# Optimization experiments

Hardware: AMD Instinct MI355X
Metric: run time of the kernel (lower is better)

Reference implementation:

```python
import jax, jax.numpy as jnp
import numpy as np

B, N, H, F = 4, 256, 192, 64
SUP = 1.0  # ancestor_suppression_strength
EPS = 1e-6


def setup_inputs() -> dict:
    key = jax.random.key(0)
    ks = jax.random.split(key, 14)
    z = jax.random.normal(ks[0], (B, H), jnp.float32)
    # strictly-lower-triangular 0/1 parent (link) matrix: row t lists parents j < t
    tri = jnp.tril(jnp.ones((N, N), jnp.float32), -1)
    targets = (jax.random.uniform(ks[1], (B, N, N)) < 0.05).astype(jnp.float32) * tri

    def w(k, shape):
        fan_in = shape[0]
        return jax.random.normal(k, shape, jnp.float32) / jnp.sqrt(jnp.float32(fan_in))

    return {
        "z": z,
        "teacher_forcing_targets": targets,
        "W_init": w(ks[2], (H, H)), "b_init": jnp.zeros((H,), jnp.float32),
        "W_ih": w(ks[3], (H, 3 * H)), "W_hh": w(ks[4], (H, 3 * H)),
        "b_ih": jnp.zeros((3 * H,), jnp.float32), "b_hh": jnp.zeros((3 * H,), jnp.float32),
        "W1": w(ks[5], (3 * H, H)), "b1": jnp.zeros((H,), jnp.float32),
        "W2": w(ks[6], (H, 1)), "b2": jnp.zeros((1,), jnp.float32),
        "Wf": w(ks[7], (H, F)), "bf": jnp.zeros((F,), jnp.float32),
        "atom_count": N,
    }


def gru_cell(x, h, W_ih, W_hh, b_ih, b_hh):
    gx = x @ W_ih + b_ih
    gh = h @ W_hh + b_hh
    xr, xu, xn = jnp.split(gx, 3, axis=-1)
    hr, hu, hn = jnp.split(gh, 3, axis=-1)
    r = jax.nn.sigmoid(xr + hr)
    u = jax.nn.sigmoid(xu + hu)
    n = jnp.tanh(xn + r * hn)
    return (1.0 - u) * n + u * h


def reference(z, teacher_forcing_targets, W_init, b_init, W_ih, W_hh, b_ih, b_hh,
              W1, b1, W2, b2, Wf, bf, atom_count):
    b, n = teacher_forcing_targets.shape[0], teacher_forcing_targets.shape[1]
    h = z.shape[-1]
    idx = jnp.arange(n)

    # decoder_init: latent z -> hidden state of node 0
    h0 = jnp.tanh(z @ W_init + b_init)
    S0 = jnp.zeros((b, n, h), z.dtype).at[:, 0].set(h0)   # node states
    A0 = jnp.zeros((b, n, n), z.dtype)                    # ancestor indicator A[b,i,j]=1 iff j ancestor of i

    def step(carry, xs):
        S, A, ll = carry
        t, tgt = xs                                   # t scalar, tgt (B,N) = parents of node t
        mask = (idx < t).astype(S.dtype)              # existing nodes
        cnt = jnp.maximum(mask.sum(), 1.0)
        # mean-aggregation over existing node states -> GRU message
        m = (S * mask[None, :, None]).sum(axis=1) / cnt              # (B,H)
        h_prov = gru_cell(m, z, W_ih, W_hh, b_ih, b_hh)              # provisional state of new node
        # parent logits: MLP([h_new, h_existing, z]) per candidate parent
        feats = jnp.concatenate([
            jnp.broadcast_to(h_prov[:, None, :], S.shape), S,
            jnp.broadcast_to(z[:, None, :], S.shape)], axis=-1)      # (B,N,3H)
        logits = (jax.nn.relu(feats @ W1 + b1) @ W2 + b2)[..., 0]    # (B,N)
        # ancestor suppression: suppress j if j is already an ancestor of one of t's parents
        reach = jnp.einsum('bn,bnm->bm', tgt, A)
        anc = (reach > 0).astype(S.dtype)
        p = jax.nn.sigmoid(logits) * (1.0 - SUP * anc)
        p = jnp.clip(p, EPS, 1.0 - EPS)
        ll = ll + (mask[None, :] * (tgt * jnp.log(p) + (1.0 - tgt) * jnp.log1p(-p))).sum()
        # teacher forcing: commit parents, update new-node state from parent states
        deg = jnp.maximum(tgt.sum(axis=-1, keepdims=True), 1.0)
        msg = jnp.einsum('bn,bnh->bh', tgt, S) / deg
        h_new = gru_cell(msg, h_prov, W_ih, W_hh, b_ih, b_hh)
        S = jax.lax.dynamic_update_slice(S, h_new[:, None, :], (0, t, 0))
        row = jnp.minimum(tgt + anc, 1.0)             # ancestors(t) = parents U ancestors(parents)
        A = jax.lax.dynamic_update_slice(A, row[:, None, :], (0, t, 0))
        return (S, A, ll), None

    ts = jnp.arange(1, n)
    tgt_rows = jnp.swapaxes(teacher_forcing_targets[:, 1:, :], 0, 1)  # (N-1,B,N)
    (S, A, ll), _ = jax.lax.scan(step, (S0, A0, jnp.zeros((), z.dtype)), (ts, tgt_rows))

    L = teacher_forcing_targets            # teacher-forced link matrix
    node_features = S @ Wf + bf            # node_feature_decoder head
    return L, node_features, ll
```

## Files before the change

kernel.cpp:

```cpp
#include <hip/hip_runtime.h>
#include <stdint.h>

#define B_ 4
#define N_ 256
#define H_ 192
#define H3_ 576
#define F_ 64
#define SH_ 12
#define SC_ 36

#define H0_OFF   0u
#define ZC_OFF   1024u
#define HL_OFF   2048u
#define SL_OFF   395264u
#define AN_OFF   788480u
#define TG_OFF   796672u
#define PL_OFF   804864u
#define PC_OFF   870400u
#define DG_OFF   871424u
#define G_OFF    872448u
#define C_OFF    1069056u
#define CL_OFF   1265664u
#define CC_OFF   1331200u
#define XC_OFF   1332224u
#define FHL_OFF  1332288u
#define FSL_OFF  1725504u

#define AN64 (AN_OFF/2)
#define TG64 (TG_OFF/2)

#define NF_OUT 262144u
#define LL_OUT 327680u

__device__ __forceinline__ float sigm_(float x){ return 1.0f/(1.0f + __expf(-x)); }
__device__ __forceinline__ float tanh_(float x){
  float ax = fabsf(x);
  float e = __expf(-2.0f*ax);
  float t = (1.0f - e)/(1.0f + e);
  return x < 0.0f ? -t : t;
}

__device__ __forceinline__ void st_mall_(uint32_t* p, unsigned long long u){
  __hip_atomic_store((unsigned long long*)p, u, __ATOMIC_RELAXED, __HIP_MEMORY_SCOPE_AGENT);
}
__device__ __forceinline__ unsigned long long ld_mall_(const uint32_t* p){
  return __hip_atomic_load((const unsigned long long*)p, __ATOMIC_RELAXED, __HIP_MEMORY_SCOPE_AGENT);
}
__device__ __forceinline__ unsigned long long ld_l2_(const uint32_t* p){
  unsigned long long v;
  asm volatile("buffer_inv sc0\n\t"
               "s_waitcnt vmcnt(0)\n\t"
               "global_load_dwordx2 %0, %1, off\n\t"
               "s_waitcnt vmcnt(0)"
               : "=v"(v) : "v"(p) : "memory");
  return v;
}
__device__ __forceinline__ void pub_(uint32_t* fp, uint32_t* mp, float v, uint32_t tag){
  unsigned long long u = ((unsigned long long)tag<<32) | (unsigned long long)__float_as_uint(v);
  __hip_atomic_store((unsigned long long*)fp, u, __ATOMIC_RELAXED, __HIP_MEMORY_SCOPE_WORKGROUP);
  st_mall_(mp, u);
}
__device__ __forceinline__ float pollH_(const uint32_t* fp, const uint32_t* mp, int fast, uint32_t tag){
  unsigned long long x = 0; int it = 0;
  for(;;){
    if (fast){
      x = ld_l2_(fp);
      if ((uint32_t)(x>>32) != tag && (((++it) & 3) == 3)){
        unsigned long long m = ld_mall_(mp);
        if ((uint32_t)(m>>32) == tag) x = m;
      }
    } else {
      x = ld_mall_(mp);
    }
    if (__all((int)((uint32_t)(x>>32) == tag))) break;
  }
  return __uint_as_float((uint32_t)x);
}

__global__ void __launch_bounds__(192) k_pre1(const float* __restrict__ z,
    const float* __restrict__ Winit, const float* __restrict__ binit,
    const float* __restrict__ W1, const float* __restrict__ b1,
    const float* __restrict__ tgt, float* ws, float* out)
{
  int bx = blockIdx.x, b = blockIdx.y, tid = threadIdx.x;
  if (bx == N_){
    __shared__ float zs[H_];
    zs[tid] = z[b*H_ + tid];
    __syncthreads();
    float a0=0.f, a1=0.f;
    for (int k=0;k<H_;k++){
      float zv = zs[k];
      a0 += zv * Winit[(size_t)k*H_ + tid];
      a1 += zv * W1[(size_t)(2*H_ + k)*H_ + tid];
    }
    ws[H0_OFF + b*H_ + tid] = tanh_(a0 + binit[tid]);
    ws[ZC_OFF + b*H_ + tid] = a1 + b1[tid];
    if (b==0 && tid==0) out[LL_OUT] = 0.0f;
    return;
  }
  if (tid >= 64) return;
  int t = bx, lane = tid;
  uint32_t* wsu = (uint32_t*)ws;
  unsigned long long* ws64 = (unsigned long long*)ws;
  const float* row = tgt + ((size_t)(b*N_) + t)*N_;
  uint8_t* pl = ((uint8_t*)&wsu[PL_OFF]) + (size_t)(b*N_ + t)*N_;
  int cnt = 0;
  #pragma unroll
  for (int m=0;m<4;m++){
    float v = row[m*64 + lane];
    bool p = (v != 0.0f);
    unsigned long long bw = __ballot(p);
    if (lane == 0) ws64[TG64 + (size_t)(b*N_+t)*4 + m] = bw;
    if (p){
      int pos = cnt + (int)__popcll(bw & ((1ULL<<lane)-1ULL));
      pl[pos] = (uint8_t)(m*64 + lane);
    }
    cnt += (int)__popcll(bw);
  }
  if (lane == 0){
    wsu[PC_OFF + b*N_ + t] = (uint32_t)cnt;
    ws[DG_OFF + b*N_ + t] = 1.0f / fmaxf((float)cnt, 1.0f);
  }
}

__global__ void __launch_bounds__(64) k_pre2(float* ws)
{
  int j = blockIdx.x, b = blockIdx.y, lane = threadIdx.x;
  uint32_t* wsu = (uint32_t*)ws;
  unsigned long long* ws64 = (unsigned long long*)ws;
  uint8_t* cl = ((uint8_t*)&wsu[CL_OFF]) + (size_t)(b*N_ + j)*N_;
  int w = j >> 6; int sb = j & 63;
  int cnt = 0;
  #pragma unroll
  for (int m=0;m<4;m++){
    int t = m*64 + lane;
    unsigned long long rowm = ws64[TG64 + (size_t)(b*N_+t)*4 + w];
    bool p = ((rowm >> sb) & 1ULL) != 0ULL;
    unsigned long long bw = __ballot(p);
    if (p){
      int pos = cnt + (int)__popcll(bw & ((1ULL<<lane)-1ULL));
      cl[pos] = (uint8_t)t;
    }
    cnt += (int)__popcll(bw);
  }
  if (lane == 0) wsu[CC_OFF + b*N_ + j] = (uint32_t)cnt;
}

__global__ void __launch_bounds__(256) k_pass1(const float* __restrict__ z,
    const float* __restrict__ Wih, const float* __restrict__ Whh,
    const float* __restrict__ bih_g, const float* __restrict__ bhh_g,
    float* ws)
{
  int bx = blockIdx.x;
  int b = bx & 7;
  if (b >= B_) return;
  int slice = bx >> 3;
  int tid = threadIdx.x;
  float* wsf = ws;
  uint32_t* wsu = (uint32_t*)ws;
  unsigned long long* ws64 = (unsigned long long*)ws;

  __shared__ __align__(16) float sruns[H_];
  __shared__ __align__(16) float sh[H_];
  __shared__ __align__(16) float sPS[N_*SC_];
  __shared__ __align__(16) float sdelta[2][SC_];
  __shared__ int sfast[16];
  __shared__ unsigned long long sAB[N_][4];
  __shared__ float sDG[N_], sTF1[N_], sTF2[N_];

  const int hh = tid >> 4;
  const int kc = tid & 15;
  const bool mv = tid < 192;

  uint32_t xcc = (uint32_t)__builtin_amdgcn_s_getreg((31u<<11) | 20u) & 15u;
  if (tid == 0)
    __hip_atomic_store(&wsu[XC_OFF + b*16 + slice], 0xC0DE0000u | xcc,
                       __ATOMIC_RELAXED, __HIP_MEMORY_SCOPE_AGENT);
  if (tid < 64){
    uint32_t v = 0; int ok;
    do {
      v = (tid < 16) ? __hip_atomic_load(&wsu[XC_OFF + b*16 + tid],
              __ATOMIC_RELAXED, __HIP_MEMORY_SCOPE_AGENT) : 0xC0DE0000u;
      ok = (int)((v >> 16) == 0xC0DEu);
    } while (!__all(ok));
    if (tid < 16) sfast[tid] = ((v & 0xFFu) == xcc) ? 1 : 0;
  }

  for (int i = tid; i < N_; i += 256){
    sDG[i] = wsf[DG_OFF + b*N_ + i];
    float f1 = 0.f, f2 = 0.f;
    if (i >= 1){
      unsigned long long w1 = ws64[TG64 + (size_t)(b*N_+i)*4 + ((i-1)>>6)];
      f1 = (float)((w1 >> ((i-1)&63)) & 1ULL);
    }
    if (i >= 2){
      unsigned long long w2 = ws64[TG64 + (size_t)(b*N_+i)*4 + ((i-2)>>6)];
      f2 = (float)((w2 >> ((i-2)&63)) & 1ULL);
    }
    sTF1[i] = f1; sTF2[i] = f2;
  }

  float rwih[3][12], rwhh[3][12], rbih[3], rbhh[3], rghz[3];
  if (mv){
    #pragma unroll
    for (int g=0; g<3; g++){
      int col = g*H_ + slice*SH_ + hh;
      #pragma unroll
      for (int i=0;i<12;i++){
        rwih[g][i] = Wih[(size_t)(kc*12+i)*H3_ + col];
        rwhh[g][i] = Whh[(size_t)(kc*12+i)*H3_ + col];
      }
      rbih[g] = bih_g[col];
      rbhh[g] = bhh_g[col];
    }
    float a0=0.f,a1=0.f,a2=0.f;
    #pragma unroll
    for (int i=0;i<12;i++){
      float zv = z[b*H_ + kc*12 + i];
      a0 += zv*rwhh[0][i]; a1 += zv*rwhh[1][i]; a2 += zv*rwhh[2][i];
    }
    #pragma unroll
    for (int m=1;m<16;m<<=1){
      a0 += __shfl_xor(a0,m); a1 += __shfl_xor(a1,m); a2 += __shfl_xor(a2,m);
    }
    rghz[0]=a0+rbhh[0]; rghz[1]=a1+rbhh[1]; rghz[2]=a2+rbhh[2];
  }
  float zreg = mv ? z[b*H_ + slice*SH_ + hh] : 0.0f;
  for (int i = tid; i < N_*SC_; i += 256) sPS[i] = 0.0f;
  if (tid >= 192 && tid < 196) sAB[0][tid-192] = 0ULL;
  if (mv && kc == 0){
    float v = wsf[H0_OFF + b*H_ + slice*SH_ + hh];
    int e = slice*SH_ + hh;
    pub_(&wsu[FSL_OFF + (unsigned)(b*N_)*384u + 2u*e],
         &wsu[SL_OFF  + (unsigned)(b*N_)*384u + 2u*e], v, 1u);
  }
  __syncthreads();

  const int fastf = mv ? sfast[tid/12] : 0;
  float rsum = 0.f;
  float qp0=0.f,qp1=0.f,qp2=0.f, dp0=0.f,dp1=0.f,dp2=0.f;

  for (int t=1; t<N_; t++){
    const uint32_t tagS = (uint32_t)t;
    const uint32_t tagH = (uint32_t)(t+1);
    if (mv){
      float v = pollH_(&wsu[FSL_OFF + (unsigned)(b*N_+(t-1))*384u + 2u*(unsigned)tid],
                       &wsu[SL_OFF  + (unsigned)(b*N_+(t-1))*384u + 2u*(unsigned)tid],
                       fastf, tagS);
      rsum += v;
      sruns[tid] = rsum;
    }
    __syncthreads();
    float hp=0.f, a20=0.f, a21=0.f, a22=0.f;
    if (mv){
      float dginv = sDG[t], tf1 = sTF1[t], tf2 = sTF2[t];
      float x[12];
      *(float4*)&x[0] = *(float4*)&sruns[kc*12];
      *(float4*)&x[4] = *(float4*)&sruns[kc*12+4];
      *(float4*)&x[8] = *(float4*)&sruns[kc*12+8];
      float q0=0.f,q1=0.f,q2=0.f;
      #pragma unroll
      for (int i=0;i<12;i++){
        q0 += x[i]*rwih[0][i]; q1 += x[i]*rwih[1][i]; q2 += x[i]*rwih[2][i];
      }
      #pragma unroll
      for (int m=1;m<16;m<<=1){
        q0 += __shfl_xor(q0,m); q1 += __shfl_xor(q1,m); q2 += __shfl_xor(q2,m);
      }
      float d0=q0-qp0, d1=q1-qp1, d2=q2-qp2;
      qp0=q0; qp1=q1; qp2=q2;
      if (kc == 0){
        sdelta[t&1][0*12+hh]=d0; sdelta[t&1][1*12+hh]=d1; sdelta[t&1][2*12+hh]=d2;
      }
      float pv0 = sPS[t*SC_ + 0*12 + hh];
      float pv1 = sPS[t*SC_ + 1*12 + hh];
      float pv2 = sPS[t*SC_ + 2*12 + hh];
      a20 = (pv0 + tf1*d0 + tf2*dp0)*dginv + rbih[0];
      a21 = (pv1 + tf1*d1 + tf2*dp1)*dginv + rbih[1];
      a22 = (pv2 + tf1*d2 + tf2*dp2)*dginv + rbih[2];
      dp0=d0; dp1=d1; dp2=d2;
      float invt = 1.0f/(float)t;
      float a10 = q0*invt + rbih[0];
      float a11 = q1*invt + rbih[1];
      float a12 = q2*invt + rbih[2];
      float r = sigm_(a10 + rghz[0]);
      float u = sigm_(a11 + rghz[1]);
      float n = tanh_(a12 + r*rghz[2]);
      hp = (1.0f-u)*n + u*zreg;
      if (kc == 0){
        int e = slice*SH_ + hh;
        pub_(&wsu[FHL_OFF + (unsigned)(b*N_+t)*384u + 2u*e],
             &wsu[HL_OFF  + (unsigned)(b*N_+t)*384u + 2u*e], hp, tagH);
      }
      float hv = pollH_(&wsu[FHL_OFF + (unsigned)(b*N_+t)*384u + 2u*(unsigned)tid],
                        &wsu[HL_OFF  + (unsigned)(b*N_+t)*384u + 2u*(unsigned)tid],
                        fastf, tagH);
      sh[tid] = hv;
    } else {
      int lane = tid - 192;
      if (lane < SC_){
        if (t >= 2){
          int node = t-2;
          int ccn = (int)wsu[CC_OFF + b*N_ + node];
          const uint8_t* cl = ((const uint8_t*)&wsu[CL_OFF]) + (size_t)(b*N_ + node)*N_;
          float dd = sdelta[(t-1)&1][lane];
          for (int i=0;i<ccn;i++){
            int tc = cl[i];
            if (tc > t) sPS[tc*SC_ + lane] += dd;
          }
        }
      } else if (lane < SC_+4){
        int w = lane - SC_;
        int npt = (int)wsu[PC_OFF + b*N_ + t];
        const uint8_t* pb = ((const uint8_t*)&wsu[PL_OFF]) + (size_t)(b*N_ + t)*N_;
        unsigned long long acc = 0ULL;
        for (int i=0;i<npt;i++) acc |= sAB[pb[i]][w];
        if (slice == 0) ws64[AN64 + (size_t)(b*N_+t)*4 + w] = acc;
        sAB[t][w] = acc | ws64[TG64 + (size_t)(b*N_+t)*4 + w];
      }
    }
    __syncthreads();
    if (mv){
      float x[12];
      *(float4*)&x[0] = *(float4*)&sh[kc*12];
      *(float4*)&x[4] = *(float4*)&sh[kc*12+4];
      *(float4*)&x[8] = *(float4*)&sh[kc*12+8];
      float y0=0.f,y1=0.f,y2=0.f;
      #pragma unroll
      for (int i=0;i<12;i++){
        y0 += x[i]*rwhh[0][i]; y1 += x[i]*rwhh[1][i]; y2 += x[i]*rwhh[2][i];
      }
      #pragma unroll
      for (int m=1;m<16;m<<=1){
        y0 += __shfl_xor(y0,m); y1 += __shfl_xor(y1,m); y2 += __shfl_xor(y2,m);
      }
      float r2 = sigm_(a20 + y0 + rbhh[0]);
      float u2 = sigm_(a21 + y1 + rbhh[1]);
      float n2 = tanh_(a22 + r2*(y2 + rbhh[2]));
      float hn = (1.0f-u2)*n2 + u2*hp;
      if (kc == 0){
        int e = slice*SH_ + hh;
        pub_(&wsu[FSL_OFF + (unsigned)(b*N_+t)*384u + 2u*e],
             &wsu[SL_OFF  + (unsigned)(b*N_+t)*384u + 2u*e], hn, tagH);
      }
    }
  }
}

__global__ void k_p2a(const float* __restrict__ W1, const float* __restrict__ Wf,
    const float* __restrict__ bf, float* ws, float* out)
{
  int j = blockIdx.x, b = blockIdx.y, tid = threadIdx.x;
  __shared__ float srow[H_], hrow[H_];
  __shared__ float nfp[3][F_];
  srow[tid] = ws[SL_OFF + (unsigned)(b*N_+j)*384u + 2u*tid];
  hrow[tid] = ws[HL_OFF + (unsigned)(b*N_+j)*384u + 2u*tid];
  __syncthreads();
  float accG = 0.f, accC = 0.f;
  for (int k=0;k<H_;k++){
    float sv = srow[k], hv = hrow[k];
    accG += sv * W1[(size_t)(H_+k)*H_ + tid];
    accC += hv * W1[(size_t)k*H_ + tid];
  }
  ws[G_OFF + ((size_t)b*H_ + tid)*N_ + j] = accG;
  ws[C_OFF + (size_t)(b*N_+j)*H_ + tid] = accC + ws[ZC_OFF + b*H_ + tid];
  int f = tid & 63, kp = tid >> 6;
  float a = 0.f;
  for (int i=0;i<64;i++){ int k = kp*64 + i; a += srow[k]*Wf[(size_t)k*F_ + f]; }
  nfp[kp][f] = a;
  __syncthreads();
  if (tid < F_) out[NF_OUT + (size_t)(b*N_+j)*F_ + tid] = nfp[0][tid]+nfp[1][tid]+nfp[2][tid] + bf[tid];
}

__global__ void __launch_bounds__(256) k_p2b(const float* __restrict__ W2,
    const float* __restrict__ b2p, float* ws, float* out)
{
  int t = blockIdx.x + 1, b = blockIdx.y;
  int tid = threadIdx.x; int lane = tid & 63; int wv = tid >> 6;
  __shared__ float cv[H_], w2s[H_];
  __shared__ float wsum[4];
  unsigned long long* ws64 = (unsigned long long*)ws;
  if (tid < H_){
    cv[tid] = ws[C_OFF + (size_t)(b*N_+t)*H_ + tid];
    w2s[tid] = W2[tid];
  }
  __syncthreads();
  float acc = 0.f;
  if (tid < t){
    const float* GT = ws + G_OFF + (size_t)b*H_*N_;
    float a = 0.f;
    for (int k=0;k<H_;k++) a += fmaxf(cv[k] + GT[(size_t)k*N_ + tid], 0.f) * w2s[k];
    float logit = a + b2p[0];
    float pp = 1.0f/(1.0f+__expf(-logit));
    unsigned long long an = ws64[AN64 + (size_t)(b*N_+t)*4 + (tid>>6)];
    unsigned long long tg = ws64[TG64 + (size_t)(b*N_+t)*4 + (tid>>6)];
    float anc = (float)((an >> (tid&63)) & 1ULL);
    pp = pp * (1.0f - anc);
    pp = fminf(fmaxf(pp, 1e-6f), 1.0f - 1e-6f);
    int tgb = (int)((tg >> (tid&63)) & 1ULL);
    acc = tgb ? logf(pp) : log1pf(-pp);
  }
  #pragma unroll
  for (int m=32;m>=1;m>>=1) acc += __shfl_xor(acc, m);
  if (lane == 0) wsum[wv] = acc;
  __syncthreads();
  if (tid == 0) atomicAdd(out + LL_OUT, wsum[0]+wsum[1]+wsum[2]+wsum[3]);
}

extern "C" void kernel_launch(void* const* d_in, const int* in_sizes, int n_in,
                              void* d_out, int out_size, void* d_ws, size_t ws_size,
                              hipStream_t stream) {
  (void)in_sizes; (void)n_in; (void)out_size; (void)ws_size;
  const float* z     = (const float*)d_in[0];
  const float* tgt   = (const float*)d_in[1];
  const float* Winit = (const float*)d_in[2];
  const float* binit = (const float*)d_in[3];
  const float* Wih   = (const float*)d_in[4];
  const float* Whh   = (const float*)d_in[5];
  const float* bih   = (const float*)d_in[6];
  const float* bhh   = (const float*)d_in[7];
  const float* W1    = (const float*)d_in[8];
  const float* b1    = (const float*)d_in[9];
  const float* W2    = (const float*)d_in[10];
  const float* b2    = (const float*)d_in[11];
  const float* Wf    = (const float*)d_in[12];
  const float* bf    = (const float*)d_in[13];
  float* out = (float*)d_out;
  float* ws  = (float*)d_ws;

  hipMemcpyAsync(d_out, d_in[1], (size_t)B_*N_*N_*sizeof(float), hipMemcpyDeviceToDevice, stream);

  k_pre1<<<dim3(N_+1, B_), dim3(192), 0, stream>>>(z, Winit, binit, W1, b1, tgt, ws, out);
  k_pre2<<<dim3(N_, B_), dim3(64), 0, stream>>>(ws);
  k_pass1<<<dim3(128), dim3(256), 0, stream>>>(z, Wih, Whh, bih, bhh, ws);
  k_p2a<<<dim3(N_, B_), dim3(H_), 0, stream>>>(W1, Wf, bf, ws, out);
  k_p2b<<<dim3(N_-1, B_), dim3(256), 0, stream>>>(W2, b2, ws, out);
}
```

Before: 930.0 us.

## Repartition GRU recurrence across three blocks per batch with per-step delta gather

The sequential recurrence kernel goes from 16 blocks per batch element (12 hidden units each, 256 threads) to 3 blocks per batch element (64 hidden units each, 512 threads), which cuts the number of blocks that must exchange state through global memory every step. The old scatter of prefix-sum deltas into shared memory, and the k_pre2 child-list kernel that fed it, are removed. In their place each step writes its delta rows to global memory, and the parent-message term is built by gathering those rows over the parent list. Each block now publishes and polls only the other blocks' slices, and the ancestor OR-reduction is split across 16 lanes. The cost is more registers per thread (24-wide weight slices), a per-step global gather over parents, and fewer CUs doing the serial work.

```diff
diff --git a/kernel.cpp b/kernel.cpp
--- a/kernel.cpp
+++ b/kernel.cpp
@@ -6,8 +6,6 @@
 #define H_ 192
 #define H3_ 576
 #define F_ 64
-#define SH_ 12
-#define SC_ 36
 
 #define H0_OFF   0u
 #define ZC_OFF   1024u
@@ -18,13 +16,12 @@
 #define PL_OFF   804864u
 #define PC_OFF   870400u
 #define DG_OFF   871424u
-#define G_OFF    872448u
-#define C_OFF    1069056u
-#define CL_OFF   1265664u
-#define CC_OFF   1331200u
-#define XC_OFF   1332224u
-#define FHL_OFF  1332288u
-#define FSL_OFF  1725504u
+#define D_OFF    872448u
+#define G_OFF    1462272u
+#define C_OFF    1658880u
+#define FHL_OFF  1855488u
+#define FSL_OFF  2248704u
+#define XC_OFF   2641920u
 
 #define AN64 (AN_OFF/2)
 #define TG64 (TG_OFF/2)
@@ -123,30 +120,7 @@
   }
 }
 
-__global__ void __launch_bounds__(64) k_pre2(float* ws)
-{
-  int j = blockIdx.x, b = blockIdx.y, lane = threadIdx.x;
-  uint32_t* wsu = (uint32_t*)ws;
-  unsigned long long* ws64 = (unsigned long long*)ws;
-  uint8_t* cl = ((uint8_t*)&wsu[CL_OFF]) + (size_t)(b*N_ + j)*N_;
-  int w = j >> 6; int sb = j & 63;
-  int cnt = 0;
-  #pragma unroll
-  for (int m=0;m<4;m++){
-    int t = m*64 + lane;
-    unsigned long long rowm = ws64[TG64 + (size_t)(b*N_+t)*4 + w];
-    bool p = ((rowm >> sb) & 1ULL) != 0ULL;
-    unsigned long long bw = __ballot(p);
-    if (p){
-      int pos = cnt + (int)__popcll(bw & ((1ULL<<lane)-1ULL));
-      cl[pos] = (uint8_t)t;
-    }
-    cnt += (int)__popcll(bw);
-  }
-  if (lane == 0) wsu[CC_OFF + b*N_ + j] = (uint32_t)cnt;
-}
-
-__global__ void __launch_bounds__(256) k_pass1(const float* __restrict__ z,
+__global__ void __launch_bounds__(512, 2) k_pass1(const float* __restrict__ z,
     const float* __restrict__ Wih, const float* __restrict__ Whh,
     const float* __restrict__ bih_g, const float* __restrict__ bhh_g,
     float* ws)
@@ -154,196 +128,194 @@
   int bx = blockIdx.x;
   int b = bx & 7;
   if (b >= B_) return;
-  int slice = bx >> 3;
+  int blk = bx >> 3;
   int tid = threadIdx.x;
+  const int e  = tid >> 3;
+  const int kc = tid & 7;
+  const int E  = blk*64 + e;
+
   float* wsf = ws;
   uint32_t* wsu = (uint32_t*)ws;
   unsigned long long* ws64 = (unsigned long long*)ws;
 
-  __shared__ __align__(16) float sruns[H_];
   __shared__ __align__(16) float sh[H_];
-  __shared__ __align__(16) float sPS[N_*SC_];
-  __shared__ __align__(16) float sdelta[2][SC_];
-  __shared__ int sfast[16];
+  __shared__ __align__(16) float ss[H_];
+  __shared__ float sDG[N_], sTF1[N_];
+  __shared__ uint32_t sPC[N_];
+  __shared__ int sfast[4];
   __shared__ unsigned long long sAB[N_][4];
-  __shared__ float sDG[N_], sTF1[N_], sTF2[N_];
-
-  const int hh = tid >> 4;
-  const int kc = tid & 15;
-  const bool mv = tid < 192;
+
+  {
+    float v = wsf[H0_OFF + b*H_ + E];
+    if (kc == 0)
+      pub_(&wsu[FSL_OFF + (unsigned)(b*N_)*384u + 2u*(unsigned)E],
+           &wsu[SL_OFF  + (unsigned)(b*N_)*384u + 2u*(unsigned)E], v, 1u);
+    if (kc == 1) ss[E] = v;
+  }
 
   uint32_t xcc = (uint32_t)__builtin_amdgcn_s_getreg((31u<<11) | 20u) & 15u;
   if (tid == 0)
-    __hip_atomic_store(&wsu[XC_OFF + b*16 + slice], 0xC0DE0000u | xcc,
+    __hip_atomic_store(&wsu[XC_OFF + b*16 + blk], 0xC0DE0000u | xcc,
                        __ATOMIC_RELAXED, __HIP_MEMORY_SCOPE_AGENT);
   if (tid < 64){
     uint32_t v = 0; int ok;
     do {
-      v = (tid < 16) ? __hip_atomic_load(&wsu[XC_OFF + b*16 + tid],
-              __ATOMIC_RELAXED, __HIP_MEMORY_SCOPE_AGENT) : 0xC0DE0000u;
+      v = (tid < 3) ? __hip_atomic_load(&wsu[XC_OFF + b*16 + tid],
+              __ATOMIC_RELAXED, __HIP_MEMORY_SCOPE_AGENT) : (0xC0DE0000u | xcc);
       ok = (int)((v >> 16) == 0xC0DEu);
     } while (!__all(ok));
-    if (tid < 16) sfast[tid] = ((v & 0xFFu) == xcc) ? 1 : 0;
-  }
-
-  for (int i = tid; i < N_; i += 256){
+    if (tid < 3) sfast[tid] = ((v & 0xFFu) == xcc) ? 1 : 0;
+  }
+
+  for (int i = tid; i < N_; i += 512){
     sDG[i] = wsf[DG_OFF + b*N_ + i];
-    float f1 = 0.f, f2 = 0.f;
+    sPC[i] = wsu[PC_OFF + b*N_ + i];
+    float f1 = 0.f;
     if (i >= 1){
       unsigned long long w1 = ws64[TG64 + (size_t)(b*N_+i)*4 + ((i-1)>>6)];
       f1 = (float)((w1 >> ((i-1)&63)) & 1ULL);
     }
-    if (i >= 2){
-      unsigned long long w2 = ws64[TG64 + (size_t)(b*N_+i)*4 + ((i-2)>>6)];
-      f2 = (float)((w2 >> ((i-2)&63)) & 1ULL);
-    }
-    sTF1[i] = f1; sTF2[i] = f2;
-  }
-
-  float rwih[3][12], rwhh[3][12], rbih[3], rbhh[3], rghz[3];
-  if (mv){
-    #pragma unroll
-    for (int g=0; g<3; g++){
-      int col = g*H_ + slice*SH_ + hh;
-      #pragma unroll
-      for (int i=0;i<12;i++){
-        rwih[g][i] = Wih[(size_t)(kc*12+i)*H3_ + col];
-        rwhh[g][i] = Whh[(size_t)(kc*12+i)*H3_ + col];
+    sTF1[i] = f1;
+  }
+  if (blk == 0 && tid >= 192 && tid < 196) sAB[0][tid-192] = 0ULL;
+
+  float rwih[3][24], rwhh[3][24], rbih[3], rbhh[3], rghz[3];
+  #pragma unroll
+  for (int g=0; g<3; g++){
+    int col = g*H_ + E;
+    #pragma unroll
+    for (int i=0;i<24;i++){
+      rwih[g][i] = Wih[(size_t)(kc*24+i)*H3_ + col];
+      rwhh[g][i] = Whh[(size_t)(kc*24+i)*H3_ + col];
+    }
+    rbih[g] = bih_g[col];
+    rbhh[g] = bhh_g[col];
+  }
+  {
+    float a0=0.f,a1=0.f,a2=0.f;
+    #pragma unroll
+    for (int i=0;i<24;i++){
+      float zv = z[b*H_ + kc*24 + i];
+      a0 += zv*rwhh[0][i]; a1 += zv*rwhh[1][i]; a2 += zv*rwhh[2][i];
+    }
+    #pragma unroll
+    for (int m=1;m<8;m<<=1){
+      a0 += __shfl_xor(a0,m); a1 += __shfl_xor(a1,m); a2 += __shfl_xor(a2,m);
+    }
+    rghz[0]=a0+rbhh[0]; rghz[1]=a1+rbhh[1]; rghz[2]=a2+rbhh[2];
+  }
+  float zreg = z[b*H_ + E];
+
+  __syncthreads();
+  if (tid < 128){
+    int j = (tid < blk*64) ? tid : tid + 64;
+    ss[j] = pollH_(&wsu[FSL_OFF + (unsigned)(b*N_)*384u + 2u*(unsigned)j],
+                   &wsu[SL_OFF  + (unsigned)(b*N_)*384u + 2u*(unsigned)j],
+                   sfast[j>>6], 1u);
+  }
+  __syncthreads();
+
+  float q0=0.f, q1=0.f, q2=0.f;
+  const uint8_t* plbase = ((const uint8_t*)&wsu[PL_OFF]) + (size_t)(b*N_)*N_;
+  float* Dbase = wsf + D_OFF + (size_t)((b*3+blk)*N_)*H_;
+
+  for (int t=1; t<N_; t++){
+    const uint32_t tagH = (uint32_t)(t+1);
+    float d0=0.f,d1=0.f,d2=0.f;
+    #pragma unroll
+    for (int c=0;c<6;c++){
+      float4 v4 = *(const float4*)&ss[kc*24 + c*4];
+      float xx0=v4.x, xx1=v4.y, xx2=v4.z, xx3=v4.w;
+      d0 += xx0*rwih[0][c*4+0]; d1 += xx0*rwih[1][c*4+0]; d2 += xx0*rwih[2][c*4+0];
+      d0 += xx1*rwih[0][c*4+1]; d1 += xx1*rwih[1][c*4+1]; d2 += xx1*rwih[2][c*4+1];
+      d0 += xx2*rwih[0][c*4+2]; d1 += xx2*rwih[1][c*4+2]; d2 += xx2*rwih[2][c*4+2];
+      d0 += xx3*rwih[0][c*4+3]; d1 += xx3*rwih[1][c*4+3]; d2 += xx3*rwih[2][c*4+3];
+    }
+    #pragma unroll
+    for (int m=1;m<8;m<<=1){
+      d0 += __shfl_xor(d0,m); d1 += __shfl_xor(d1,m); d2 += __shfl_xor(d2,m);
+    }
+    q0 += d0; q1 += d1; q2 += d2;
+    float invt = 1.0f/(float)t;
+    float r = sigm_(q0*invt + rbih[0] + rghz[0]);
+    float u = sigm_(q1*invt + rbih[1] + rghz[1]);
+    float n = tanh_(q2*invt + rbih[2] + r*rghz[2]);
+    float hp = (1.0f-u)*n + u*zreg;
+    if (kc == 0){
+      pub_(&wsu[FHL_OFF + (unsigned)(b*N_+t)*384u + 2u*(unsigned)E],
+           &wsu[HL_OFF  + (unsigned)(b*N_+t)*384u + 2u*(unsigned)E], hp, tagH);
+      float* Dr = Dbase + (size_t)(t-1)*H_;
+      Dr[e] = d0; Dr[64+e] = d1; Dr[128+e] = d2;
+    }
+    if (kc == 1) sh[E] = hp;
+    float ga0=0.f, ga1=0.f, ga2=0.f;
+    {
+      int pc = (int)sPC[t];
+      const uint8_t* pl = plbase + (size_t)t*N_;
+      for (int i=kc; i<pc; i+=8){
+        int p = pl[i];
+        if (p == t-1) continue;
+        const float* Dp = Dbase + (size_t)p*H_;
+        ga0 += Dp[e]; ga1 += Dp[64+e]; ga2 += Dp[128+e];
       }
-      rbih[g] = bih_g[col];
-      rbhh[g] = bhh_g[col];
-    }
-    float a0=0.f,a1=0.f,a2=0.f;
-    #pragma unroll
-    for (int i=0;i<12;i++){
-      float zv = z[b*H_ + kc*12 + i];
-      a0 += zv*rwhh[0][i]; a1 += zv*rwhh[1][i]; a2 += zv*rwhh[2][i];
-    }
-    #pragma unroll
-    for (int m=1;m<16;m<<=1){
-      a0 += __shfl_xor(a0,m); a1 += __shfl_xor(a1,m); a2 += __shfl_xor(a2,m);
-    }
-    rghz[0]=a0+rbhh[0]; rghz[1]=a1+rbhh[1]; rghz[2]=a2+rbhh[2];
-  }
-  float zreg = mv ? z[b*H_ + slice*SH_ + hh] : 0.0f;
-  for (int i = tid; i < N_*SC_; i += 256) sPS[i] = 0.0f;
-  if (tid >= 192 && tid < 196) sAB[0][tid-192] = 0ULL;
-  if (mv && kc == 0){
-    float v = wsf[H0_OFF + b*H_ + slice*SH_ + hh];
-    int e = slice*SH_ + hh;
-    pub_(&wsu[FSL_OFF + (unsigned)(b*N_)*384u + 2u*e],
-         &wsu[SL_OFF  + (unsigned)(b*N_)*384u + 2u*e], v, 1u);
-  }
-  __syncthreads();
-
-  const int fastf = mv ? sfast[tid/12] : 0;
-  float rsum = 0.f;
-  float qp0=0.f,qp1=0.f,qp2=0.f, dp0=0.f,dp1=0.f,dp2=0.f;
-
-  for (int t=1; t<N_; t++){
-    const uint32_t tagS = (uint32_t)t;
-    const uint32_t tagH = (uint32_t)(t+1);
-    if (mv){
-      float v = pollH_(&wsu[FSL_OFF + (unsigned)(b*N_+(t-1))*384u + 2u*(unsigned)tid],
-                       &wsu[SL_OFF  + (unsigned)(b*N_+(t-1))*384u + 2u*(unsigned)tid],
-                       fastf, tagS);
-      rsum += v;
-      sruns[tid] = rsum;
-    }
-    __syncthreads();
-    float hp=0.f, a20=0.f, a21=0.f, a22=0.f;
-    if (mv){
-      float dginv = sDG[t], tf1 = sTF1[t], tf2 = sTF2[t];
-      float x[12];
-      *(float4*)&x[0] = *(float4*)&sruns[kc*12];
-      *(float4*)&x[4] = *(float4*)&sruns[kc*12+4];
-      *(float4*)&x[8] = *(float4*)&sruns[kc*12+8];
-      float q0=0.f,q1=0.f,q2=0.f;
-      #pragma unroll
-      for (int i=0;i<12;i++){
-        q0 += x[i]*rwih[0][i]; q1 += x[i]*rwih[1][i]; q2 += x[i]*rwih[2][i];
-      }
-      #pragma unroll
-      for (int m=1;m<16;m<<=1){
-        q0 += __shfl_xor(q0,m); q1 += __shfl_xor(q1,m); q2 += __shfl_xor(q2,m);
-      }
-      float d0=q0-qp0, d1=q1-qp1, d2=q2-qp2;
-      qp0=q0; qp1=q1; qp2=q2;
-      if (kc == 0){
-        sdelta[t&1][0*12+hh]=d0; sdelta[t&1][1*12+hh]=d1; sdelta[t&1][2*12+hh]=d2;
-      }
-      float pv0 = sPS[t*SC_ + 0*12 + hh];
-      float pv1 = sPS[t*SC_ + 1*12 + hh];
-      float pv2 = sPS[t*SC_ + 2*12 + hh];
-      a20 = (pv0 + tf1*d0 + tf2*dp0)*dginv + rbih[0];
-      a21 = (pv1 + tf1*d1 + tf2*dp1)*dginv + rbih[1];
-      a22 = (pv2 + tf1*d2 + tf2*dp2)*dginv + rbih[2];
-      dp0=d0; dp1=d1; dp2=d2;
-      float invt = 1.0f/(float)t;
-      float a10 = q0*invt + rbih[0];
-      float a11 = q1*invt + rbih[1];
-      float a12 = q2*invt + rbih[2];
-      float r = sigm_(a10 + rghz[0]);
-      float u = sigm_(a11 + rghz[1]);
-      float n = tanh_(a12 + r*rghz[2]);
-      hp = (1.0f-u)*n + u*zreg;
-      if (kc == 0){
-        int e = slice*SH_ + hh;
-        pub_(&wsu[FHL_OFF + (unsigned)(b*N_+t)*384u + 2u*e],
-             &wsu[HL_OFF  + (unsigned)(b*N_+t)*384u + 2u*e], hp, tagH);
-      }
-      float hv = pollH_(&wsu[FHL_OFF + (unsigned)(b*N_+t)*384u + 2u*(unsigned)tid],
-                        &wsu[HL_OFF  + (unsigned)(b*N_+t)*384u + 2u*(unsigned)tid],
-                        fastf, tagH);
-      sh[tid] = hv;
-    } else {
-      int lane = tid - 192;
-      if (lane < SC_){
-        if (t >= 2){
-          int node = t-2;
-          int ccn = (int)wsu[CC_OFF + b*N_ + node];
-          const uint8_t* cl = ((const uint8_t*)&wsu[CL_OFF]) + (size_t)(b*N_ + node)*N_;
-          float dd = sdelta[(t-1)&1][lane];
-          for (int i=0;i<ccn;i++){
-            int tc = cl[i];
-            if (tc > t) sPS[tc*SC_ + lane] += dd;
-          }
-        }
-      } else if (lane < SC_+4){
-        int w = lane - SC_;
-        int npt = (int)wsu[PC_OFF + b*N_ + t];
-        const uint8_t* pb = ((const uint8_t*)&wsu[PL_OFF]) + (size_t)(b*N_ + t)*N_;
-        unsigned long long acc = 0ULL;
-        for (int i=0;i<npt;i++) acc |= sAB[pb[i]][w];
-        if (slice == 0) ws64[AN64 + (size_t)(b*N_+t)*4 + w] = acc;
+    }
+    #pragma unroll
+    for (int m=1;m<8;m<<=1){
+      ga0 += __shfl_xor(ga0,m); ga1 += __shfl_xor(ga1,m); ga2 += __shfl_xor(ga2,m);
+    }
+    if (tid < 128){
+      int j = (tid < blk*64) ? tid : tid + 64;
+      sh[j] = pollH_(&wsu[FHL_OFF + (unsigned)(b*N_+t)*384u + 2u*(unsigned)j],
+                     &wsu[HL_OFF  + (unsigned)(b*N_+t)*384u + 2u*(unsigned)j],
+                     sfast[j>>6], tagH);
+    } else if (blk == 0 && tid >= 192 && tid < 208){
+      int lane16 = tid - 192;
+      int ip = lane16 >> 2, w = lane16 & 3;
+      int pc = (int)sPC[t];
+      const uint8_t* pl = plbase + (size_t)t*N_;
+      unsigned long long acc = 0ULL;
+      for (int i=ip; i<pc; i+=4) acc |= sAB[pl[i]][w];
+      acc |= __shfl_xor(acc, 4);
+      acc |= __shfl_xor(acc, 8);
+      if (ip == 0){
+        ws64[AN64 + (size_t)(b*N_+t)*4 + w] = acc;
         sAB[t][w] = acc | ws64[TG64 + (size_t)(b*N_+t)*4 + w];
       }
     }
     __syncthreads();
-    if (mv){
-      float x[12];
-      *(float4*)&x[0] = *(float4*)&sh[kc*12];
-      *(float4*)&x[4] = *(float4*)&sh[kc*12+4];
-      *(float4*)&x[8] = *(float4*)&sh[kc*12+8];
-      float y0=0.f,y1=0.f,y2=0.f;
-      #pragma unroll
-      for (int i=0;i<12;i++){
-        y0 += x[i]*rwhh[0][i]; y1 += x[i]*rwhh[1][i]; y2 += x[i]*rwhh[2][i];
-      }
-      #pragma unroll
-      for (int m=1;m<16;m<<=1){
-        y0 += __shfl_xor(y0,m); y1 += __shfl_xor(y1,m); y2 += __shfl_xor(y2,m);
-      }
-      float r2 = sigm_(a20 + y0 + rbhh[0]);
-      float u2 = sigm_(a21 + y1 + rbhh[1]);
-      float n2 = tanh_(a22 + r2*(y2 + rbhh[2]));
-      float hn = (1.0f-u2)*n2 + u2*hp;
-      if (kc == 0){
-        int e = slice*SH_ + hh;
-        pub_(&wsu[FSL_OFF + (unsigned)(b*N_+t)*384u + 2u*e],
-             &wsu[SL_OFF  + (unsigned)(b*N_+t)*384u + 2u*e], hn, tagH);
-      }
-    }
+    float y0=0.f,y1=0.f,y2=0.f;
+    #pragma unroll
+    for (int c=0;c<6;c++){
+      float4 v4 = *(const float4*)&sh[kc*24 + c*4];
+      float xx0=v4.x, xx1=v4.y, xx2=v4.z, xx3=v4.w;
+      y0 += xx0*rwhh[0][c*4+0]; y1 += xx0*rwhh[1][c*4+0]; y2 += xx0*rwhh[2][c*4+0];
+      y0 += xx1*rwhh[0][c*4+1]; y1 += xx1*rwhh[1][c*4+1]; y2 += xx1*rwhh[2][c*4+1];
+      y0 += xx2*rwhh[0][c*4+2]; y1 += xx2*rwhh[1][c*4+2]; y2 += xx2*rwhh[2][c*4+2];
+      y0 += xx3*rwhh[0][c*4+3]; y1 += xx3*rwhh[1][c*4+3]; y2 += xx3*rwhh[2][c*4+3];
+    }
+    #pragma unroll
+    for (int m=1;m<8;m<<=1){
+      y0 += __shfl_xor(y0,m); y1 += __shfl_xor(y1,m); y2 += __shfl_xor(y2,m);
+    }
+    float dginv = sDG[t], tf1 = sTF1[t];
+    float gxa = (ga0 + tf1*d0)*dginv + rbih[0];
+    float gxb = (ga1 + tf1*d1)*dginv + rbih[1];
+    float gxc = (ga2 + tf1*d2)*dginv + rbih[2];
+    float r2 = sigm_(gxa + y0 + rbhh[0]);
+    float u2 = sigm_(gxb + y1 + rbhh[1]);
+    float n2 = tanh_(gxc + r2*(y2 + rbhh[2]));
+    float hn = (1.0f-u2)*n2 + u2*hp;
+    if (kc == 0)
+      pub_(&wsu[FSL_OFF + (unsigned)(b*N_+t)*384u + 2u*(unsigned)E],
+           &wsu[SL_OFF  + (unsigned)(b*N_+t)*384u + 2u*(unsigned)E], hn, tagH);
+    if (kc == 1) ss[E] = hn;
+    if (tid < 128){
+      int j = (tid < blk*64) ? tid : tid + 64;
+      ss[j] = pollH_(&wsu[FSL_OFF + (unsigned)(b*N_+t)*384u + 2u*(unsigned)j],
+                     &wsu[SL_OFF  + (unsigned)(b*N_+t)*384u + 2u*(unsigned)j],
+                     sfast[j>>6], tagH);
+    }
+    __syncthreads();
   }
 }
 
@@ -431,8 +403,7 @@
   hipMemcpyAsync(d_out, d_in[1], (size_t)B_*N_*N_*sizeof(float), hipMemcpyDeviceToDevice, stream);
 
   k_pre1<<<dim3(N_+1, B_), dim3(192), 0, stream>>>(z, Winit, binit, W1, b1, tgt, ws, out);
-  k_pre2<<<dim3(N_, B_), dim3(64), 0, stream>>>(ws);
-  k_pass1<<<dim3(128), dim3(256), 0, stream>>>(z, Wih, Whh, bih, bhh, ws);
+  k_pass1<<<dim3(24), dim3(512), 0, stream>>>(z, Wih, Whh, bih, bhh, ws);
   k_p2a<<<dim3(N_, B_), dim3(H_), 0, stream>>>(W1, Wf, bf, ws, out);
   k_p2b<<<dim3(N_-1, B_), dim3(256), 0, stream>>>(W2, b2, ws, out);
 }
```

After: 938.0 us. About the same (+0.9%).
